# Performance work log

Measured on AMD Instinct MI355X. Metric: run time of the kernel, lower is better.

Reference implementation:

```python
import jax, jax.numpy as jnp
import numpy as np

NUM_HEADS = 16


def setup_inputs() -> dict:
    key = jax.random.key(0)
    k1, k2, k3, k4 = jax.random.split(key, 4)
    B, S, E = 2, 2048, 1024
    x = jax.random.normal(k1, (B, S, E), dtype=jnp.float32)
    src_padding_mask = jax.random.randint(k2, (B, S), 0, 2) > 0  # True = keep
    # xavier-uniform-ish scale for linear weights (shape (out, in), torch convention)
    w_qkv = jax.random.normal(k3, (3 * E, E), dtype=jnp.float32) * (1.0 / np.sqrt(E))
    w_o = jax.random.normal(k4, (E, E), dtype=jnp.float32) * (1.0 / np.sqrt(E))
    return {"x": x, "src_padding_mask": src_padding_mask, "w_qkv": w_qkv, "w_o": w_o}


def reference(x, src_padding_mask, w_qkv, w_o):
    B, S, E = x.shape
    H = NUM_HEADS
    D = E // H
    # fused qkv projection: (B,S,3E) -> (B,S,H,3D) -> split
    qkv = jnp.einsum("bse,fe->bsf", x, w_qkv).reshape(B, S, H, 3 * D)
    q, k, v = jnp.split(qkv, 3, axis=-1)
    # (B,H,S,D)
    q = q.transpose(0, 2, 1, 3)
    k = k.transpose(0, 2, 1, 3)
    v = v.transpose(0, 2, 1, 3)
    logits = jnp.einsum("bhqd,bhkd->bhqk", q, k) / jnp.sqrt(jnp.float32(D))
    logits = jnp.where(src_padding_mask[:, None, None, :], logits, -jnp.inf)
    attn = jax.nn.softmax(logits, axis=-1)
    values = jnp.einsum("bhqk,bhkd->bhqd", attn, v)  # (B,H,S,D)
    values = values.transpose(0, 2, 1, 3).reshape(B, S, E)
    out = jnp.einsum("bse,fe->bsf", values, w_o)
    return out
```

## Files before the change

kernel.cpp:

```cpp
#include <hip/hip_runtime.h>
#include <hip/hip_bf16.h>

#define B_NUM 2
#define S_LEN 2048
#define E_DIM 1024
#define H_NUM 16
#define D_DIM 64
#define QKV_LD 3072
#define QSCALE_LOG2E 0.18033688011112042f

typedef __attribute__((ext_vector_type(8))) short bf16x8;
typedef __attribute__((ext_vector_type(8))) unsigned short u16x8;
typedef __attribute__((ext_vector_type(4))) unsigned short u16x4;
typedef __attribute__((ext_vector_type(4))) float f32x4;
typedef __attribute__((ext_vector_type(16))) float f32x16;
typedef __attribute__((ext_vector_type(2))) int i32x2;

static __device__ __forceinline__ unsigned short f2bf(float f) {
    union { float f; unsigned int u; } v; v.f = f;
    unsigned int r = v.u + 0x7fffu + ((v.u >> 16) & 1u);
    return (unsigned short)(r >> 16);
}

static __device__ __forceinline__ unsigned cvtpk_bf16(float lo, float hi) {
    unsigned r;
    asm("v_cvt_pk_bf16_f32 %0, %1, %2" : "=v"(r) : "v"(lo), "v"(hi));
    return r;
}

static __device__ __forceinline__ void gload16(const void* gsrc, void* ldst) {
    __builtin_amdgcn_global_load_lds(
        (const __attribute__((address_space(1))) unsigned int*)gsrc,
        (__attribute__((address_space(3))) unsigned int*)ldst, 16, 0, 0);
}

__global__ __launch_bounds__(256)
void cvt_f32_bf16(const float* __restrict__ in, unsigned short* __restrict__ outp, int n4) {
    int i = blockIdx.x * blockDim.x + threadIdx.x;
    if (i < n4) {
        float4 f = ((const float4*)in)[i];
        u16x4 o = { f2bf(f.x), f2bf(f.y), f2bf(f.z), f2bf(f.w) };
        ((u16x4*)outp)[i] = o;
    }
}

template <bool OUT_BF16, bool QSCALE>
__global__ __launch_bounds__(256)
void gemm_bt_mfma128(const unsigned short* __restrict__ A,
                     const unsigned short* __restrict__ Bw,
                     void* __restrict__ Cv, int M, int N, int K) {
    __shared__ unsigned short As[128 * 64];
    __shared__ unsigned short Bs[128 * 64];
    char* const AsB = (char*)As;
    char* const BsB = (char*)Bs;
    const int tid  = threadIdx.x;
    const int lane = tid & 63;
    const int w    = tid >> 6;
    const int lg   = lane >> 4;
    const int lq   = lane & 15;
    const int bm = blockIdx.y * 128;
    const int bn = blockIdx.x * 128;
    const int wr = (w >> 1) * 64;
    const int wc = (w & 1) * 64;
    const int lrow8 = lane >> 3;
    const int gblk  = (lane & 7) ^ lrow8;

    f32x4 acc[4][4];
#pragma unroll
    for (int i = 0; i < 4; ++i)
#pragma unroll
        for (int j = 0; j < 4; ++j) acc[i][j] = (f32x4){0.f, 0.f, 0.f, 0.f};

    for (int k0 = 0; k0 < K; k0 += 64) {
        __syncthreads();
#pragma unroll
        for (int t = 0; t < 4; ++t) {
            const int c = w * 4 + t;
            const int row = c * 8 + lrow8;
            gload16(A + (size_t)(bm + row) * K + k0 + gblk * 8, AsB + c * 1024);
            gload16(Bw + (size_t)(bn + row) * K + k0 + gblk * 8, BsB + c * 1024);
        }
        __syncthreads();

        bf16x8 af[4][2], bfr[4][2];
#pragma unroll
        for (int rt = 0; rt < 4; ++rt) {
            const int row = wr + rt * 16 + lq;
            const int sz = (row & 7) << 4;
            af[rt][0] = *(const bf16x8*)(AsB + row * 128 + ((lg * 16)      ^ sz));
            af[rt][1] = *(const bf16x8*)(AsB + row * 128 + ((64 + lg * 16) ^ sz));
        }
#pragma unroll
        for (int ct = 0; ct < 4; ++ct) {
            const int row = wc + ct * 16 + lq;
            const int sz = (row & 7) << 4;
            bfr[ct][0] = *(const bf16x8*)(BsB + row * 128 + ((lg * 16)      ^ sz));
            bfr[ct][1] = *(const bf16x8*)(BsB + row * 128 + ((64 + lg * 16) ^ sz));
        }
#pragma unroll
        for (int rt = 0; rt < 4; ++rt)
#pragma unroll
            for (int ct = 0; ct < 4; ++ct) {
                acc[rt][ct] = __builtin_amdgcn_mfma_f32_16x16x32_bf16(af[rt][0], bfr[ct][0], acc[rt][ct], 0, 0, 0);
                acc[rt][ct] = __builtin_amdgcn_mfma_f32_16x16x32_bf16(af[rt][1], bfr[ct][1], acc[rt][ct], 0, 0, 0);
            }
    }

#pragma unroll
    for (int rt = 0; rt < 4; ++rt)
#pragma unroll
        for (int ct = 0; ct < 4; ++ct) {
            const int row = bm + wr + rt * 16 + lg * 4;
            const int col = bn + wc + ct * 16 + lq;
            float scale = 1.f;
            if constexpr (QSCALE) scale = ((col % 192) < 64) ? QSCALE_LOG2E : 1.f;
#pragma unroll
            for (int r = 0; r < 4; ++r) {
                float vv = acc[rt][ct][r] * scale;
                if constexpr (OUT_BF16)
                    ((unsigned short*)Cv)[(size_t)(row + r) * N + col] = f2bf(vv);
                else
                    ((float*)Cv)[(size_t)(row + r) * N + col] = vv;
            }
        }
}

template <bool OUT_BF16, bool QSCALE>
__global__ __launch_bounds__(256)
void gemm_bt_mfma(const unsigned short* __restrict__ A,
                  const unsigned short* __restrict__ Bw,
                  void* __restrict__ Cv, int M, int N, int K) {
    __shared__ unsigned short As[64 * 64];
    __shared__ unsigned short Bs[64 * 64];
    char* const AsB = (char*)As;
    char* const BsB = (char*)Bs;
    const int tid  = threadIdx.x;
    const int lane = tid & 63;
    const int w    = tid >> 6;
    const int lg   = lane >> 4;
    const int lq   = lane & 15;
    const int bm = blockIdx.y * 64;
    const int bn = blockIdx.x * 64;
    const int wr = (w >> 1) * 32;
    const int wc = (w & 1) * 32;
    const int sr = tid >> 2;
    const int sc = (tid & 3) * 16;
    const int swzS = (sr & 7) << 4;

    f32x4 acc[2][2];
#pragma unroll
    for (int i = 0; i < 2; ++i)
#pragma unroll
        for (int j = 0; j < 2; ++j) acc[i][j] = (f32x4){0.f, 0.f, 0.f, 0.f};

    const unsigned short* ap = A  + (size_t)(bm + sr) * K + sc;
    const unsigned short* bp = Bw + (size_t)(bn + sr) * K + sc;

    for (int k0 = 0; k0 < K; k0 += 64) {
        __syncthreads();
        u16x8 av0 = *(const u16x8*)(ap + k0);
        u16x8 av1 = *(const u16x8*)(ap + k0 + 8);
        u16x8 bv0 = *(const u16x8*)(bp + k0);
        u16x8 bv1 = *(const u16x8*)(bp + k0 + 8);
        *(u16x8*)(AsB + sr * 128 + ((sc * 2)      ^ swzS)) = av0;
        *(u16x8*)(AsB + sr * 128 + ((sc * 2 + 16) ^ swzS)) = av1;
        *(u16x8*)(BsB + sr * 128 + ((sc * 2)      ^ swzS)) = bv0;
        *(u16x8*)(BsB + sr * 128 + ((sc * 2 + 16) ^ swzS)) = bv1;
        __syncthreads();

        bf16x8 af[2][2], bfr[2][2];
#pragma unroll
        for (int rt = 0; rt < 2; ++rt) {
            const int row = wr + rt * 16 + lq;
            const int sz = (row & 7) << 4;
            af[rt][0] = *(const bf16x8*)(AsB + row * 128 + ((lg * 16)      ^ sz));
            af[rt][1] = *(const bf16x8*)(AsB + row * 128 + ((64 + lg * 16) ^ sz));
        }
#pragma unroll
        for (int ct = 0; ct < 2; ++ct) {
            const int row = wc + ct * 16 + lq;
            const int sz = (row & 7) << 4;
            bfr[ct][0] = *(const bf16x8*)(BsB + row * 128 + ((lg * 16)      ^ sz));
            bfr[ct][1] = *(const bf16x8*)(BsB + row * 128 + ((64 + lg * 16) ^ sz));
        }
#pragma unroll
        for (int rt = 0; rt < 2; ++rt)
#pragma unroll
            for (int ct = 0; ct < 2; ++ct) {
                acc[rt][ct] = __builtin_amdgcn_mfma_f32_16x16x32_bf16(af[rt][0], bfr[ct][0], acc[rt][ct], 0, 0, 0);
                acc[rt][ct] = __builtin_amdgcn_mfma_f32_16x16x32_bf16(af[rt][1], bfr[ct][1], acc[rt][ct], 0, 0, 0);
            }
    }

#pragma unroll
    for (int rt = 0; rt < 2; ++rt)
#pragma unroll
        for (int ct = 0; ct < 2; ++ct) {
            const int row = bm + wr + rt * 16 + lg * 4;
            const int col = bn + wc + ct * 16 + lq;
            float scale = 1.f;
            if constexpr (QSCALE) scale = ((col % 192) < 64) ? QSCALE_LOG2E : 1.f;
#pragma unroll
            for (int r = 0; r < 4; ++r) {
                float vv = acc[rt][ct][r] * scale;
                if constexpr (OUT_BF16)
                    ((unsigned short*)Cv)[(size_t)(row + r) * N + col] = f2bf(vv);
                else
                    ((float*)Cv)[(size_t)(row + r) * N + col] = vv;
            }
        }
}

__global__ __launch_bounds__(256)
void attn_v7(const unsigned short* __restrict__ qkv, const int* __restrict__ mask,
             unsigned short* __restrict__ vout) {
    __shared__ __align__(16) char KsP[3][8192];
    __shared__ __align__(16) char VtP[2][8192];
    __shared__ __align__(16) float BiasF[S_LEN];

    const int tid  = threadIdx.x;
    const int lane = tid & 63;
    const int w    = tid >> 6;
    const int ln   = lane & 31;
    const int hi   = lane >> 5;
    const int q0 = blockIdx.x * 128;
    const int h  = blockIdx.y;
    const int b  = blockIdx.z;
    const size_t baseBH = (size_t)b * S_LEN * QKV_LD + (size_t)h * (3 * D_DIM);
    const unsigned short* const kv = qkv + baseBH;

    {
        const int4* mr = (const int4*)(mask + (size_t)b * S_LEN);
        int4 m0 = mr[tid * 2];
        int4 m1 = mr[tid * 2 + 1];
        float4 f0 = { m0.x ? 0.f : -30000.f, m0.y ? 0.f : -30000.f,
                      m0.z ? 0.f : -30000.f, m0.w ? 0.f : -30000.f };
        float4 f1 = { m1.x ? 0.f : -30000.f, m1.y ? 0.f : -30000.f,
                      m1.z ? 0.f : -30000.f, m1.w ? 0.f : -30000.f };
        ((float4*)BiasF)[tid * 2]     = f0;
        ((float4*)BiasF)[tid * 2 + 1] = f1;
    }

    bf16x8 qf[4];
    {
        const unsigned short* qp = kv + (size_t)(q0 + w * 32 + ln) * QKV_LD + hi * 8;
#pragma unroll
        for (int kk = 0; kk < 4; ++kk)
            qf[kk] = *(const bf16x8*)(qp + kk * 16);
    }

    const int lrow8 = lane >> 3;
    const int gblk  = (lane & 7) ^ lrow8;
    const int vkb = (tid & 15) * 4;
    const int vdb = (tid >> 4) * 4;

    {
#pragma unroll
        for (int t = 0; t < 2; ++t) {
            const int c = w * 2 + t;
            gload16(kv + (size_t)(c * 8 + lrow8) * QKV_LD + D_DIM + gblk * 8,
                    KsP[0] + c * 1024);
            gload16(kv + (size_t)(64 + c * 8 + lrow8) * QKV_LD + D_DIM + gblk * 8,
                    KsP[1] + c * 1024);
        }
        u16x4 vr[4];
#pragma unroll
        for (int i = 0; i < 4; ++i)
            vr[i] = *(const u16x4*)(kv + (size_t)(vkb + i) * QKV_LD + 2 * D_DIM + vdb);
#pragma unroll
        for (int j = 0; j < 4; ++j) {
            u16x4 o = { vr[0][j], vr[1][j], vr[2][j], vr[3][j] };
            const int row = vdb + j;
            *(u16x4*)(VtP[0] + row * 128 + ((vkb * 2) ^ ((row & 7) << 4))) = o;
        }
    }
    __builtin_amdgcn_sched_barrier(0);
    asm volatile("s_waitcnt vmcnt(0) lgkmcnt(0)" ::: "memory");
    __builtin_amdgcn_s_barrier();
    __builtin_amdgcn_sched_barrier(0);

    f32x16 accO[2];
#pragma unroll
    for (int dt = 0; dt < 2; ++dt)
#pragma unroll
        for (int r = 0; r < 16; ++r) accO[dt][r] = 0.f;
    f32x4 rsumv = (f32x4){0.f, 0.f, 0.f, 0.f};

    const int NT = S_LEN / 64;
    int cur3 = 0;
    int k2b  = 2;
    for (int it = 0; it < NT; ++it) {
        const int curv = it & 1;
        const int kv0 = it * 64;
        char* const KsC = KsP[cur3];
        char* const VtC = VtP[curv];
        const bool pfV = (it + 1 < NT);
        const bool pfK = (it + 2 < NT);

        u16x4 vr[4];
        if (pfV) {
            const int kvn = kv0 + 64;
#pragma unroll
            for (int i = 0; i < 4; ++i)
                vr[i] = *(const u16x4*)(kv + (size_t)(kvn + vkb + i) * QKV_LD + 2 * D_DIM + vdb);
        }
        if (pfK) {
            const int kvn2 = kv0 + 128;
#pragma unroll
            for (int t = 0; t < 2; ++t) {
                const int c = w * 2 + t;
                gload16(kv + (size_t)(kvn2 + c * 8 + lrow8) * QKV_LD + D_DIM + gblk * 8,
                        KsP[k2b] + c * 1024);
            }
        }

        f32x16 s[2];
#pragma unroll
        for (int ks = 0; ks < 2; ++ks)
#pragma unroll
            for (int m = 0; m < 4; ++m) {
                f32x4 b4 = *(const f32x4*)(&BiasF[kv0 + ks * 32 + m * 8 + hi * 4]);
#pragma unroll
                for (int i = 0; i < 4; ++i) s[ks][m * 4 + i] = b4[i];
            }
        __builtin_amdgcn_s_setprio(1);
#pragma unroll
        for (int ks = 0; ks < 2; ++ks) {
            const int krow = ks * 32 + ln;
            const int swz = (ln & 7) << 4;
#pragma unroll
            for (int kk = 0; kk < 4; ++kk) {
                bf16x8 kf = *(const bf16x8*)(KsC + krow * 128 + (((kk * 16 + hi * 8) * 2) ^ swz));
                s[ks] = __builtin_amdgcn_mfma_f32_32x32x16_bf16(kf, qf[kk], s[ks], 0, 0, 0);
            }
        }
        __builtin_amdgcn_s_setprio(0);

#pragma unroll
        for (int ks = 0; ks < 2; ++ks)
#pragma unroll
            for (int r = 0; r < 16; ++r) {
                float p = __builtin_amdgcn_exp2f(s[ks][r]);
                s[ks][r] = p;
                rsumv[r & 3] += p;
            }

        bf16x8 pb[4];
#pragma unroll
        for (int ks = 0; ks < 2; ++ks) {
            unsigned wA[4], wB[4];
#pragma unroll
            for (int m = 0; m < 4; ++m) {
                wA[m] = cvtpk_bf16(s[ks][4 * m + 0], s[ks][4 * m + 1]);
                wB[m] = cvtpk_bf16(s[ks][4 * m + 2], s[ks][4 * m + 3]);
            }
#pragma unroll
            for (int t = 0; t < 2; ++t) {
                i32x2 ra = __builtin_amdgcn_permlane32_swap((int)wA[2 * t], (int)wA[2 * t + 1], false, false);
                i32x2 rb = __builtin_amdgcn_permlane32_swap((int)wB[2 * t], (int)wB[2 * t + 1], false, false);
                union { unsigned u[4]; bf16x8 v; } uu;
                uu.u[0] = (unsigned)ra[0];
                uu.u[1] = (unsigned)rb[0];
                uu.u[2] = (unsigned)ra[1];
                uu.u[3] = (unsigned)rb[1];
                pb[ks * 2 + t] = uu.v;
            }
        }

        __builtin_amdgcn_s_setprio(1);
#pragma unroll
        for (int dt = 0; dt < 2; ++dt) {
            const int drow = dt * 32 + ln;
            const int swz = (ln & 7) << 4;
#pragma unroll
            for (int n = 0; n < 4; ++n) {
                bf16x8 va = *(const bf16x8*)(VtC + drow * 128 + (((n * 16 + hi * 8) * 2) ^ swz));
                accO[dt] = __builtin_amdgcn_mfma_f32_32x32x16_bf16(va, pb[n], accO[dt], 0, 0, 0);
            }
        }
        __builtin_amdgcn_s_setprio(0);

        if (pfV) {
#pragma unroll
            for (int j = 0; j < 4; ++j) {
                u16x4 o = { vr[0][j], vr[1][j], vr[2][j], vr[3][j] };
                const int row = vdb + j;
                *(u16x4*)(VtP[curv ^ 1] + row * 128 + ((vkb * 2) ^ ((row & 7) << 4))) = o;
            }
            __builtin_amdgcn_sched_barrier(0);
            asm volatile("s_waitcnt lgkmcnt(0)" ::: "memory");
            __builtin_amdgcn_s_barrier();
            __builtin_amdgcn_sched_barrier(0);
        }

        cur3 = (cur3 == 2) ? 0 : cur3 + 1;
        k2b  = (k2b  == 2) ? 0 : k2b  + 1;
    }

    float rsum = rsumv[0] + rsumv[1] + rsumv[2] + rsumv[3];
    {
        i32x2 rr = __builtin_amdgcn_permlane32_swap(__float_as_int(rsum), __float_as_int(rsum), false, false);
        rsum = __int_as_float(rr[0]) + __int_as_float(rr[1]);
    }
    const float inv = 1.f / rsum;
    unsigned short* op = vout + (size_t)(b * S_LEN + q0 + w * 32 + ln) * E_DIM + h * D_DIM;
#pragma unroll
    for (int dt = 0; dt < 2; ++dt)
#pragma unroll
        for (int m = 0; m < 4; ++m) {
            u16x4 o;
#pragma unroll
            for (int i = 0; i < 4; ++i) o[i] = f2bf(accO[dt][4 * m + i] * inv);
            *(u16x4*)(op + dt * 32 + m * 8 + hi * 4) = o;
        }
}

extern "C" void kernel_launch(void* const* d_in, const int* in_sizes, int n_in,
                              void* d_out, int out_size, void* d_ws, size_t ws_size,
                              hipStream_t stream) {
    const float* x      = (const float*)d_in[0];
    const int*   mask   = (const int*)d_in[1];
    const float* w_qkv  = (const float*)d_in[2];
    const float* w_o    = (const float*)d_in[3];
    float*       out    = (float*)d_out;

    const int M = B_NUM * S_LEN;
    unsigned short* qkvb = (unsigned short*)d_ws;
    unsigned short* vbuf = qkvb + (size_t)M * 3 * E_DIM;
    unsigned short* xb   = vbuf + (size_t)M * E_DIM;
    unsigned short* wqb  = xb   + (size_t)M * E_DIM;
    unsigned short* wob  = wqb  + (size_t)3 * E_DIM * E_DIM;

    dim3 blk(256);
    {
        int n4;
        n4 = M * E_DIM / 4;
        cvt_f32_bf16<<<dim3((n4 + 255) / 256), blk, 0, stream>>>(x, xb, n4);
        n4 = 3 * E_DIM * E_DIM / 4;
        cvt_f32_bf16<<<dim3((n4 + 255) / 256), blk, 0, stream>>>(w_qkv, wqb, n4);
        n4 = E_DIM * E_DIM / 4;
        cvt_f32_bf16<<<dim3((n4 + 255) / 256), blk, 0, stream>>>(w_o, wob, n4);
    }

    gemm_bt_mfma128<true, true><<<dim3(3 * E_DIM / 128, M / 128), blk, 0, stream>>>(
        xb, wqb, qkvb, M, 3 * E_DIM, E_DIM);

    attn_v7<<<dim3(S_LEN / 128, H_NUM, B_NUM), blk, 0, stream>>>(qkvb, mask, vbuf);

    gemm_bt_mfma<false, false><<<dim3(E_DIM / 64, M / 64), blk, 0, stream>>>(
        vbuf, wob, out, M, E_DIM, E_DIM);
}
```

Measured before the change: 125.7 us.

## Software-pipeline QK^T one tile ahead of softmax and PV in attention

Restructures the attention loop so the QK^T MFMAs for the next KV tile are issued before the exp2/convert/PV work of the current tile. A prologue computes the first tile's scores, and the loop carries them in sCur/sNext. The aim is to overlap the VALU softmax work with matrix-core work inside each wave. The cost is another set of live f32x16 score registers, which raises register pressure and may lower occupancy. The K buffer indexing is rewritten to read the next tile's ring slot.

Result: no change. 128.0 us (+1.8%).

```diff
diff --git a/kernel.cpp b/kernel.cpp
--- a/kernel.cpp
+++ b/kernel.cpp
@@ -212,8 +212,8 @@
 }
 
 __global__ __launch_bounds__(256)
-void attn_v7(const unsigned short* __restrict__ qkv, const int* __restrict__ mask,
-             unsigned short* __restrict__ vout) {
+void attn_v13(const unsigned short* __restrict__ qkv, const int* __restrict__ mask,
+              unsigned short* __restrict__ vout) {
     __shared__ __align__(16) char KsP[3][8192];
     __shared__ __align__(16) char VtP[2][8192];
     __shared__ __align__(16) float BiasF[S_LEN];
@@ -226,8 +226,8 @@
     const int q0 = blockIdx.x * 128;
     const int h  = blockIdx.y;
     const int b  = blockIdx.z;
-    const size_t baseBH = (size_t)b * S_LEN * QKV_LD + (size_t)h * (3 * D_DIM);
-    const unsigned short* const kv = qkv + baseBH;
+    const unsigned short* const kv =
+        qkv + (size_t)b * S_LEN * QKV_LD + (size_t)h * (3 * D_DIM);
 
     {
         const int4* mr = (const int4*)(mask + (size_t)b * S_LEN);
@@ -286,24 +286,36 @@
         for (int r = 0; r < 16; ++r) accO[dt][r] = 0.f;
     f32x4 rsumv = (f32x4){0.f, 0.f, 0.f, 0.f};
 
+    const int kswz = (ln & 7) << 4;
+
+    f32x16 sCur[2];
+#pragma unroll
+    for (int ks = 0; ks < 2; ++ks) {
+#pragma unroll
+        for (int m = 0; m < 4; ++m) {
+            f32x4 b4 = *(const f32x4*)(&BiasF[ks * 32 + m * 8 + hi * 4]);
+#pragma unroll
+            for (int i = 0; i < 4; ++i) sCur[ks][m * 4 + i] = b4[i];
+        }
+        const int krow = ks * 32 + ln;
+#pragma unroll
+        for (int kk = 0; kk < 4; ++kk) {
+            bf16x8 kf = *(const bf16x8*)(KsP[0] + krow * 128 + (((kk * 16 + hi * 8) * 2) ^ kswz));
+            sCur[ks] = __builtin_amdgcn_mfma_f32_32x32x16_bf16(kf, qf[kk], sCur[ks], 0, 0, 0);
+        }
+    }
+
     const int NT = S_LEN / 64;
     int cur3 = 0;
-    int k2b  = 2;
     for (int it = 0; it < NT; ++it) {
         const int curv = it & 1;
         const int kv0 = it * 64;
-        char* const KsC = KsP[cur3];
         char* const VtC = VtP[curv];
+        const int nxt3 = (cur3 == 2) ? 0 : cur3 + 1;
+        const int k2b  = (nxt3 == 2) ? 0 : nxt3 + 1;
         const bool pfV = (it + 1 < NT);
         const bool pfK = (it + 2 < NT);
 
-        u16x4 vr[4];
-        if (pfV) {
-            const int kvn = kv0 + 64;
-#pragma unroll
-            for (int i = 0; i < 4; ++i)
-                vr[i] = *(const u16x4*)(kv + (size_t)(kvn + vkb + i) * QKV_LD + 2 * D_DIM + vdb);
-        }
         if (pfK) {
             const int kvn2 = kv0 + 128;
 #pragma unroll
@@ -313,46 +325,52 @@
                         KsP[k2b] + c * 1024);
             }
         }
-
-        f32x16 s[2];
+        u16x4 vr[4];
+        if (pfV) {
+            const int kvn = kv0 + 64;
+#pragma unroll
+            for (int i = 0; i < 4; ++i)
+                vr[i] = *(const u16x4*)(kv + (size_t)(kvn + vkb + i) * QKV_LD + 2 * D_DIM + vdb);
+        }
+
+        f32x16 sNext[2];
+        if (pfV) {
+            const int kvn = kv0 + 64;
+            __builtin_amdgcn_s_setprio(1);
+#pragma unroll
+            for (int ks = 0; ks < 2; ++ks) {
+#pragma unroll
+                for (int m = 0; m < 4; ++m) {
+                    f32x4 b4 = *(const f32x4*)(&BiasF[kvn + ks * 32 + m * 8 + hi * 4]);
+#pragma unroll
+                    for (int i = 0; i < 4; ++i) sNext[ks][m * 4 + i] = b4[i];
+                }
+                const int krow = ks * 32 + ln;
+#pragma unroll
+                for (int kk = 0; kk < 4; ++kk) {
+                    bf16x8 kf = *(const bf16x8*)(KsP[nxt3] + krow * 128 + (((kk * 16 + hi * 8) * 2) ^ kswz));
+                    sNext[ks] = __builtin_amdgcn_mfma_f32_32x32x16_bf16(kf, qf[kk], sNext[ks], 0, 0, 0);
+                }
+            }
+            __builtin_amdgcn_s_setprio(0);
+        }
+
 #pragma unroll
         for (int ks = 0; ks < 2; ++ks)
 #pragma unroll
-            for (int m = 0; m < 4; ++m) {
-                f32x4 b4 = *(const f32x4*)(&BiasF[kv0 + ks * 32 + m * 8 + hi * 4]);
-#pragma unroll
-                for (int i = 0; i < 4; ++i) s[ks][m * 4 + i] = b4[i];
-            }
-        __builtin_amdgcn_s_setprio(1);
-#pragma unroll
-        for (int ks = 0; ks < 2; ++ks) {
-            const int krow = ks * 32 + ln;
-            const int swz = (ln & 7) << 4;
-#pragma unroll
-            for (int kk = 0; kk < 4; ++kk) {
-                bf16x8 kf = *(const bf16x8*)(KsC + krow * 128 + (((kk * 16 + hi * 8) * 2) ^ swz));
-                s[ks] = __builtin_amdgcn_mfma_f32_32x32x16_bf16(kf, qf[kk], s[ks], 0, 0, 0);
-            }
-        }
-        __builtin_amdgcn_s_setprio(0);
-
-#pragma unroll
-        for (int ks = 0; ks < 2; ++ks)
-#pragma unroll
             for (int r = 0; r < 16; ++r) {
-                float p = __builtin_amdgcn_exp2f(s[ks][r]);
-                s[ks][r] = p;
+                float p = __builtin_amdgcn_exp2f(sCur[ks][r]);
+                sCur[ks][r] = p;
                 rsumv[r & 3] += p;
             }
-
         bf16x8 pb[4];
 #pragma unroll
         for (int ks = 0; ks < 2; ++ks) {
             unsigned wA[4], wB[4];
 #pragma unroll
             for (int m = 0; m < 4; ++m) {
-                wA[m] = cvtpk_bf16(s[ks][4 * m + 0], s[ks][4 * m + 1]);
-                wB[m] = cvtpk_bf16(s[ks][4 * m + 2], s[ks][4 * m + 3]);
+                wA[m] = cvtpk_bf16(sCur[ks][4 * m + 0], sCur[ks][4 * m + 1]);
+                wB[m] = cvtpk_bf16(sCur[ks][4 * m + 2], sCur[ks][4 * m + 3]);
             }
 #pragma unroll
             for (int t = 0; t < 2; ++t) {
@@ -391,10 +409,11 @@
             asm volatile("s_waitcnt lgkmcnt(0)" ::: "memory");
             __builtin_amdgcn_s_barrier();
             __builtin_amdgcn_sched_barrier(0);
-        }
-
-        cur3 = (cur3 == 2) ? 0 : cur3 + 1;
-        k2b  = (k2b  == 2) ? 0 : k2b  + 1;
+            sCur[0] = sNext[0];
+            sCur[1] = sNext[1];
+        }
+
+        cur3 = nxt3;
     }
 
     float rsum = rsumv[0] + rsumv[1] + rsumv[2] + rsumv[3];
@@ -445,7 +464,7 @@
     gemm_bt_mfma128<true, true><<<dim3(3 * E_DIM / 128, M / 128), blk, 0, stream>>>(
         xb, wqb, qkvb, M, 3 * E_DIM, E_DIM);
 
-    attn_v7<<<dim3(S_LEN / 128, H_NUM, B_NUM), blk, 0, stream>>>(qkvb, mask, vbuf);
+    attn_v13<<<dim3(S_LEN / 128, H_NUM, B_NUM), blk, 0, stream>>>(qkvb, mask, vbuf);
 
     gemm_bt_mfma<false, false><<<dim3(E_DIM / 64, M / 64), blk, 0, stream>>>(
         vbuf, wob, out, M, E_DIM, E_DIM);
```
